# Kernel tuning notes

Measured on AMD Instinct MI355X. Metric: run time of the kernel, lower is better.

The kernel has to match this reference:

```python
import jax, jax.numpy as jnp
import numpy as np

EMBED_DIM = 1024
N_HEAD = 16
BLOCK_SIZE = 2048
B, T = 4, 2048


def setup_inputs() -> dict:
    key = jax.random.key(0)
    kx, kw, kb = jax.random.split(key, 3)
    x = jax.random.normal(kx, (B, T, EMBED_DIM), dtype=jnp.float32)
    # nn.Linear(embed_dim, 3*embed_dim): weight [3C, C], bias [3C]
    bound = 1.0 / np.sqrt(EMBED_DIM)
    W_qkv = jax.random.uniform(kw, (3 * EMBED_DIM, EMBED_DIM), dtype=jnp.float32, minval=-bound, maxval=bound)
    b_qkv = jax.random.uniform(kb, (3 * EMBED_DIM,), dtype=jnp.float32, minval=-bound, maxval=bound)
    return {"x": x, "W_qkv": W_qkv, "b_qkv": b_qkv}


def reference(x, W_qkv, b_qkv):
    Bsz, Tlen, C = x.shape
    H = N_HEAD
    hd = C // H
    qkv = x @ W_qkv.T + b_qkv  # [B, T, 3C]
    q, k, v = jnp.split(qkv, 3, axis=2)
    # [B, H, T, hd]
    q = q.reshape(Bsz, Tlen, H, hd).transpose(0, 2, 1, 3)
    k = k.reshape(Bsz, Tlen, H, hd).transpose(0, 2, 1, 3)
    v = v.reshape(Bsz, Tlen, H, hd).transpose(0, 2, 1, 3)
    att = jnp.einsum('bhqd,bhkd->bhqk', q, k) / np.sqrt(hd).astype(np.float32)
    causal = jnp.tril(jnp.ones((Tlen, Tlen), dtype=bool))
    att = jnp.where(causal[None, None, :, :], att, -jnp.inf)
    att = jax.nn.softmax(att, axis=-1)
    out = jnp.einsum('bhqk,bhkd->bhqd', att, v)  # [B, H, T, hd]
    y = out.transpose(0, 2, 1, 3).reshape(Bsz, Tlen, C)
    return y
```

## Files before the change

### kernel.cpp

```cpp
#include <hip/hip_runtime.h>


typedef unsigned short u16;
typedef short bf16x8 __attribute__((ext_vector_type(8)));
typedef float f32x4 __attribute__((ext_vector_type(4)));
typedef float f32x16 __attribute__((ext_vector_type(16)));

__device__ __forceinline__ float exp2f_hw(float x) {
  return __builtin_amdgcn_exp2f(x);
}

__device__ __forceinline__ u16 f2b(float f) {
  union { float f; unsigned u; } x; x.f = f;
  unsigned r = x.u + 0x7FFFu + ((x.u >> 16) & 1u);
  return (u16)(r >> 16);
}

__device__ __forceinline__ unsigned cvtpk(float lo, float hi_) {
  unsigned r;
  asm("v_cvt_pk_bf16_f32 %0, %1, %2" : "=v"(r) : "v"(lo), "v"(hi_));
  return r;
}

__device__ __forceinline__ void gload16(const void* g, void* l) {
  __builtin_amdgcn_global_load_lds(
      (const __attribute__((address_space(1))) unsigned*)g,
      (__attribute__((address_space(3))) unsigned*)l, 16, 0, 0);
}

__global__ void cvt_bf16(const float* __restrict__ src, u16* __restrict__ dst, int n4) {
  int i = blockIdx.x * blockDim.x + threadIdx.x;
  const int stride = gridDim.x * blockDim.x;
  for (; i < n4; i += stride) {
    float4 v = ((const float4*)src)[i];
    ushort4 o;
    o.x = f2b(v.x); o.y = f2b(v.y); o.z = f2b(v.z); o.w = f2b(v.w);
    ((ushort4*)dst)[i] = o;
  }
}

__global__ __launch_bounds__(256) void qkv_gemm(
    const u16* __restrict__ Xb, const u16* __restrict__ Wb,
    const float* __restrict__ bias,
    u16* __restrict__ qw, u16* __restrict__ kw, u16* __restrict__ vw) {
  __shared__ u16 As[8192];
  __shared__ u16 Bs[8192];
  const int tid  = threadIdx.x;
  const int lane = tid & 63;
  const int wave = tid >> 6;
  const int ln = lane & 15, hi = lane >> 4;
  const int wr = wave >> 1, wc = wave & 1;
  const int m0 = blockIdx.y * 128;
  const int n0 = blockIdx.x * 128;
  const bool vblk = (n0 >= 2048);

  const int srow = tid >> 2;
  const int scol = (tid & 3) * 8;

  f32x4 zero = {0.f, 0.f, 0.f, 0.f};
  f32x4 acc[4][4];
#pragma unroll
  for (int i = 0; i < 4; ++i)
#pragma unroll
    for (int j = 0; j < 4; ++j) acc[i][j] = zero;

  for (int k0 = 0; k0 < 1024; k0 += 64) {
    gload16(Xb + (size_t)(m0 + srow) * 1024 + k0 + scol,           (char*)As + tid * 16);
    gload16(Xb + (size_t)(m0 + 64 + srow) * 1024 + k0 + scol,      (char*)As + 4096 + tid * 16);
    gload16(Xb + (size_t)(m0 + srow) * 1024 + k0 + 32 + scol,      (char*)As + 8192 + tid * 16);
    gload16(Xb + (size_t)(m0 + 64 + srow) * 1024 + k0 + 32 + scol, (char*)As + 12288 + tid * 16);
    gload16(Wb + (size_t)(n0 + srow) * 1024 + k0 + scol,           (char*)Bs + tid * 16);
    gload16(Wb + (size_t)(n0 + 64 + srow) * 1024 + k0 + scol,      (char*)Bs + 4096 + tid * 16);
    gload16(Wb + (size_t)(n0 + srow) * 1024 + k0 + 32 + scol,      (char*)Bs + 8192 + tid * 16);
    gload16(Wb + (size_t)(n0 + 64 + srow) * 1024 + k0 + 32 + scol, (char*)Bs + 12288 + tid * 16);
    __syncthreads();

#pragma unroll
    for (int hf = 0; hf < 2; ++hf) {
      const u16* Ah = As + hf * 4096;
      const u16* Bh = Bs + hf * 4096;
      bf16x8 af[4], bfv[4];
#pragma unroll
      for (int i = 0; i < 4; ++i)
        af[i] = *(const bf16x8*)&Ah[(wr * 64 + i * 16 + ln) * 32 + hi * 8];
#pragma unroll
      for (int j = 0; j < 4; ++j)
        bfv[j] = *(const bf16x8*)&Bh[(wc * 64 + j * 16 + ln) * 32 + hi * 8];
      if (vblk) {
#pragma unroll
        for (int i = 0; i < 4; ++i)
#pragma unroll
          for (int j = 0; j < 4; ++j)
            acc[i][j] = __builtin_amdgcn_mfma_f32_16x16x32_bf16(bfv[j], af[i], acc[i][j], 0, 0, 0);
      } else {
#pragma unroll
        for (int i = 0; i < 4; ++i)
#pragma unroll
          for (int j = 0; j < 4; ++j)
            acc[i][j] = __builtin_amdgcn_mfma_f32_16x16x32_bf16(af[i], bfv[j], acc[i][j], 0, 0, 0);
      }
    }
    __syncthreads();
  }

  const int which = n0 >> 10;
  const int h = ((n0 & 1023) >> 6) + wc;
  const size_t bh = (size_t)((m0 >> 11) * 16 + h);
  const int tloc = (m0 & 2047) + wr * 64;

  if (which == 2) {
    u16* ob = vw + bh * 131072;
#pragma unroll
    for (int j = 0; j < 4; ++j) {
      float bv[4];
#pragma unroll
      for (int r = 0; r < 4; ++r) bv[r] = bias[n0 + wc * 64 + j * 16 + hi * 4 + r];
#pragma unroll
      for (int i = 0; i < 4; ++i) {
        u16* p = ob + (((tloc >> 4) + i) * 64 + j * 16 + hi * 4) * 16 + ln;
#pragma unroll
        for (int r = 0; r < 4; ++r)
          p[r * 16] = f2b(acc[i][j][r] + bv[r]);
      }
    }
  } else {
    u16* ob = (which == 0 ? qw : kw) + bh * 131072;
    const float qs = (which == 0) ? 0.1803368801111244f : 1.0f;
    const int t5 = tloc >> 5;
#pragma unroll
    for (int j = 0; j < 4; ++j) {
      const float bv = bias[n0 + wc * 64 + j * 16 + ln];
#pragma unroll
      for (int i = 0; i < 4; ++i) {
        u16* p = ob + ((t5 + (i >> 1)) * 4 + j) * 512 + ((i & 1) * 16 + hi * 4) * 16 + ln;
#pragma unroll
        for (int r = 0; r < 4; ++r)
          p[r * 16] = f2b((acc[i][j][r] + bv) * qs);
      }
    }
  }
}

__global__ __launch_bounds__(128) void attn(
    const u16* __restrict__ qw, const u16* __restrict__ kw,
    const u16* __restrict__ vw, float* __restrict__ y) {
  __shared__ float accX[2][16][64];
  __shared__ float lX[2][16][64];

  const int lane = threadIdx.x & 63;
  const int p    = threadIdx.x >> 6;
  const int l31 = lane & 31;
  const int hi  = lane >> 5;
  const int laneoff = l31 * 16 + hi * 8;

  const int bid = blockIdx.x;
  const int xcd = bid & 7;
  const int rest = bid >> 3;
  const int task = rest & 31;
  const int bh  = xcd + 8 * (rest >> 5);
  const int bb  = bh >> 4, h = bh & 15;

  const u16* qb = qw + (size_t)bh * 131072;
  const u16* kb = kw + (size_t)bh * 131072;
  const u16* vb = vw + (size_t)bh * 131072;
  float* yb = y + (size_t)bb * 2048 * 1024 + (size_t)h * 64;

  bf16x8 onesf;
#pragma unroll
  for (int j = 0; j < 8; ++j) onesf[j] = (short)0x3F80;

#pragma unroll 1
  for (int phase = 0; phase < 2; ++phase) {
    const int chunk = phase ? (63 - task) : task;
    const int q0 = chunk * 32;
    const int jtE = chunk;

    bf16x8 qf[4];
#pragma unroll
    for (int s = 0; s < 4; ++s)
      qf[s] = *(const bf16x8*)&qb[(chunk * 4 + s) * 512 + laneoff];

    f32x16 acc0, acc1, accl;
#pragma unroll
    for (int r = 0; r < 16; ++r) { acc0[r] = 0.f; acc1[r] = 0.f; accl[r] = 0.f; }

    bf16x8 kf[4];
#pragma unroll
    for (int s = 0; s < 4; ++s)
      kf[s] = *(const bf16x8*)&kb[(p * 4 + s) * 512 + laneoff];

#pragma unroll 1
    for (int jt = p; jt <= jtE; jt += 2) {
      bf16x8 vf[4];
      vf[0] = *(const bf16x8*)&vb[((jt * 2 + 0) * 64 +  0 + l31) * 16 + hi * 8];
      vf[1] = *(const bf16x8*)&vb[((jt * 2 + 0) * 64 + 32 + l31) * 16 + hi * 8];
      vf[2] = *(const bf16x8*)&vb[((jt * 2 + 1) * 64 +  0 + l31) * 16 + hi * 8];
      vf[3] = *(const bf16x8*)&vb[((jt * 2 + 1) * 64 + 32 + l31) * 16 + hi * 8];

      f32x16 st;
#pragma unroll
      for (int r = 0; r < 16; ++r) st[r] = 0.f;
#pragma unroll
      for (int s = 0; s < 4; ++s)
        st = __builtin_amdgcn_mfma_f32_32x32x16_bf16(kf[s], qf[s], st, 0, 0, 0);

      if (jt + 2 <= jtE) {
#pragma unroll
        for (int s = 0; s < 4; ++s)
          kf[s] = *(const bf16x8*)&kb[((jt + 2) * 4 + s) * 512 + laneoff];
      }

      if (jt == jtE) {
#pragma unroll
        for (int r = 0; r < 16; ++r) {
          const int crow = (r & 3) + 8 * (r >> 2) + 4 * hi;
          if (crow > l31) st[r] = -1e30f;
        }
      }

#pragma unroll
      for (int r = 0; r < 16; ++r) st[r] = exp2f_hw(fminf(st[r], 80.f));

      bf16x8 pa0, pa1;
      {
        unsigned x0 = cvtpk(st[0], st[1]),  y0 = cvtpk(st[4], st[5]);
        unsigned x1 = cvtpk(st[2], st[3]),  y1 = cvtpk(st[6], st[7]);
        auto s0 = __builtin_amdgcn_permlane32_swap(x0, y0, false, false);
        auto s1 = __builtin_amdgcn_permlane32_swap(x1, y1, false, false);
        union { unsigned w[4]; bf16x8 v; } u;
        u.w[0] = s0[0]; u.w[1] = s1[0]; u.w[2] = s0[1]; u.w[3] = s1[1];
        pa0 = u.v;
      }
      {
        unsigned x0 = cvtpk(st[8], st[9]),   y0 = cvtpk(st[12], st[13]);
        unsigned x1 = cvtpk(st[10], st[11]), y1 = cvtpk(st[14], st[15]);
        auto s0 = __builtin_amdgcn_permlane32_swap(x0, y0, false, false);
        auto s1 = __builtin_amdgcn_permlane32_swap(x1, y1, false, false);
        union { unsigned w[4]; bf16x8 v; } u;
        u.w[0] = s0[0]; u.w[1] = s1[0]; u.w[2] = s0[1]; u.w[3] = s1[1];
        pa1 = u.v;
      }

      acc0 = __builtin_amdgcn_mfma_f32_32x32x16_bf16(pa0, vf[0], acc0, 0, 0, 0);
      acc1 = __builtin_amdgcn_mfma_f32_32x32x16_bf16(pa0, vf[1], acc1, 0, 0, 0);
      accl = __builtin_amdgcn_mfma_f32_32x32x16_bf16(pa0, onesf, accl, 0, 0, 0);
      acc0 = __builtin_amdgcn_mfma_f32_32x32x16_bf16(pa1, vf[2], acc0, 0, 0, 0);
      acc1 = __builtin_amdgcn_mfma_f32_32x32x16_bf16(pa1, vf[3], acc1, 0, 0, 0);
      accl = __builtin_amdgcn_mfma_f32_32x32x16_bf16(pa1, onesf, accl, 0, 0, 0);
    }

    __syncthreads();
    if (p == 0) {
#pragma unroll
      for (int r = 0; r < 16; ++r) { accX[0][r][lane] = acc1[r]; lX[0][r][lane] = accl[r]; }
    } else {
#pragma unroll
      for (int r = 0; r < 16; ++r) { accX[1][r][lane] = acc0[r]; lX[1][r][lane] = accl[r]; }
    }
    __syncthreads();

#pragma unroll
    for (int r = 0; r < 16; ++r) {
      const int crow = (r & 3) + 8 * (r >> 2) + 4 * hi;
      const float own = (p == 0) ? acc0[r] : acc1[r];
      const float oth = accX[p ^ 1][r][lane];
      const float inv = 1.0f / (accl[r] + lX[p ^ 1][r][lane]);
      yb[(size_t)(q0 + crow) * 1024 + p * 32 + l31] = (own + oth) * inv;
    }
  }
}

extern "C" void kernel_launch(void* const* d_in, const int* in_sizes, int n_in,
                              void* d_out, int out_size, void* d_ws, size_t ws_size,
                              hipStream_t stream) {
  const float* x    = (const float*)d_in[0];
  const float* W    = (const float*)d_in[1];
  const float* bias = (const float*)d_in[2];
  float* y = (float*)d_out;

  char* ws = (char*)d_ws;
  u16* xb = (u16*)(ws);
  u16* Wb = (u16*)(ws + 16777216);
  u16* qw = (u16*)(ws + 23068672);
  u16* kw = (u16*)(ws + 39845888);
  u16* vw = (u16*)(ws + 56623104);

  cvt_bf16<<<2048, 256, 0, stream>>>(x, xb, 8388608 / 4);
  cvt_bf16<<<1024, 256, 0, stream>>>(W, Wb, 3145728 / 4);
  qkv_gemm<<<dim3(24, 64), 256, 0, stream>>>(xb, Wb, bias, qw, kw, vw);
  attn<<<2048, 128, 0, stream>>>(qw, kw, vw, y);
}
```

Before: 153.5 us.

## Process two 32-row query chunks per attention block to reuse K/V loads

The attention kernel now handles 64 query rows per phase, as two 32-row chunks A and B that share each loaded K and V tile. The grid is halved from 2048 to 1024 blocks. The goal is to halve K/V global loads per query row and give each wave more independent MFMA work to interleave. In exchange it roughly doubles accumulator register pressure, which may lower occupancy, and adds masked wasted work on the diagonal tile for chunk A.

After: 142.0 us. 7.5% less time.

```diff
diff --git a/kernel.cpp b/kernel.cpp
--- a/kernel.cpp
+++ b/kernel.cpp
@@ -26,6 +26,29 @@
   __builtin_amdgcn_global_load_lds(
       (const __attribute__((address_space(1))) unsigned*)g,
       (__attribute__((address_space(3))) unsigned*)l, 16, 0, 0);
+}
+
+__device__ __forceinline__ void packP(f32x16 st, bf16x8& pa0, bf16x8& pa1) {
+#pragma unroll
+  for (int r = 0; r < 16; ++r) st[r] = exp2f_hw(fminf(st[r], 80.f));
+  {
+    unsigned x0 = cvtpk(st[0], st[1]),  y0 = cvtpk(st[4], st[5]);
+    unsigned x1 = cvtpk(st[2], st[3]),  y1 = cvtpk(st[6], st[7]);
+    auto s0 = __builtin_amdgcn_permlane32_swap(x0, y0, false, false);
+    auto s1 = __builtin_amdgcn_permlane32_swap(x1, y1, false, false);
+    union { unsigned w[4]; bf16x8 v; } u;
+    u.w[0] = s0[0]; u.w[1] = s1[0]; u.w[2] = s0[1]; u.w[3] = s1[1];
+    pa0 = u.v;
+  }
+  {
+    unsigned x0 = cvtpk(st[8], st[9]),   y0 = cvtpk(st[12], st[13]);
+    unsigned x1 = cvtpk(st[10], st[11]), y1 = cvtpk(st[14], st[15]);
+    auto s0 = __builtin_amdgcn_permlane32_swap(x0, y0, false, false);
+    auto s1 = __builtin_amdgcn_permlane32_swap(x1, y1, false, false);
+    union { unsigned w[4]; bf16x8 v; } u;
+    u.w[0] = s0[0]; u.w[1] = s1[0]; u.w[2] = s0[1]; u.w[3] = s1[1];
+    pa1 = u.v;
+  }
 }
 
 __global__ void cvt_bf16(const float* __restrict__ src, u16* __restrict__ dst, int n4) {
@@ -144,8 +167,10 @@
 __global__ __launch_bounds__(128) void attn(
     const u16* __restrict__ qw, const u16* __restrict__ kw,
     const u16* __restrict__ vw, float* __restrict__ y) {
-  __shared__ float accX[2][16][64];
-  __shared__ float lX[2][16][64];
+  __shared__ float accXA[2][16][64];
+  __shared__ float lXA[2][16][64];
+  __shared__ float accXB[2][16][64];
+  __shared__ float lXB[2][16][64];
 
   const int lane = threadIdx.x & 63;
   const int p    = threadIdx.x >> 6;
@@ -156,8 +181,8 @@
   const int bid = blockIdx.x;
   const int xcd = bid & 7;
   const int rest = bid >> 3;
-  const int task = rest & 31;
-  const int bh  = xcd + 8 * (rest >> 5);
+  const int pr  = rest & 15;
+  const int bh  = xcd + 8 * (rest >> 4);
   const int bb  = bh >> 4, h = bh & 15;
 
   const u16* qb = qw + (size_t)bh * 131072;
@@ -171,23 +196,29 @@
 
 #pragma unroll 1
   for (int phase = 0; phase < 2; ++phase) {
-    const int chunk = phase ? (63 - task) : task;
-    const int q0 = chunk * 32;
-    const int jtE = chunk;
-
-    bf16x8 qf[4];
-#pragma unroll
-    for (int s = 0; s < 4; ++s)
-      qf[s] = *(const bf16x8*)&qb[(chunk * 4 + s) * 512 + laneoff];
-
-    f32x16 acc0, acc1, accl;
-#pragma unroll
-    for (int r = 0; r < 16; ++r) { acc0[r] = 0.f; acc1[r] = 0.f; accl[r] = 0.f; }
+    const int s  = phase ? (31 - pr) : pr;
+    const int q0 = s * 64;
+    const int cA = 2 * s, cB = 2 * s + 1;
+    const int jtE = cB;
+
+    bf16x8 qfA[4], qfB[4];
+#pragma unroll
+    for (int sb = 0; sb < 4; ++sb) {
+      qfA[sb] = *(const bf16x8*)&qb[(cA * 4 + sb) * 512 + laneoff];
+      qfB[sb] = *(const bf16x8*)&qb[(cB * 4 + sb) * 512 + laneoff];
+    }
+
+    f32x16 accA0, accA1, acclA, accB0, accB1, acclB;
+#pragma unroll
+    for (int r = 0; r < 16; ++r) {
+      accA0[r] = 0.f; accA1[r] = 0.f; acclA[r] = 0.f;
+      accB0[r] = 0.f; accB1[r] = 0.f; acclB[r] = 0.f;
+    }
 
     bf16x8 kf[4];
 #pragma unroll
-    for (int s = 0; s < 4; ++s)
-      kf[s] = *(const bf16x8*)&kb[(p * 4 + s) * 512 + laneoff];
+    for (int sb = 0; sb < 4; ++sb)
+      kf[sb] = *(const bf16x8*)&kb[(p * 4 + sb) * 512 + laneoff];
 
 #pragma unroll 1
     for (int jt = p; jt <= jtE; jt += 2) {
@@ -197,75 +228,82 @@
       vf[2] = *(const bf16x8*)&vb[((jt * 2 + 1) * 64 +  0 + l31) * 16 + hi * 8];
       vf[3] = *(const bf16x8*)&vb[((jt * 2 + 1) * 64 + 32 + l31) * 16 + hi * 8];
 
-      f32x16 st;
-#pragma unroll
-      for (int r = 0; r < 16; ++r) st[r] = 0.f;
-#pragma unroll
-      for (int s = 0; s < 4; ++s)
-        st = __builtin_amdgcn_mfma_f32_32x32x16_bf16(kf[s], qf[s], st, 0, 0, 0);
-
+      f32x16 stA, stB;
+#pragma unroll
+      for (int r = 0; r < 16; ++r) { stA[r] = 0.f; stB[r] = 0.f; }
+#pragma unroll
+      for (int sb = 0; sb < 4; ++sb) {
+        stA = __builtin_amdgcn_mfma_f32_32x32x16_bf16(kf[sb], qfA[sb], stA, 0, 0, 0);
+        stB = __builtin_amdgcn_mfma_f32_32x32x16_bf16(kf[sb], qfB[sb], stB, 0, 0, 0);
+      }
       if (jt + 2 <= jtE) {
 #pragma unroll
-        for (int s = 0; s < 4; ++s)
-          kf[s] = *(const bf16x8*)&kb[((jt + 2) * 4 + s) * 512 + laneoff];
-      }
-
-      if (jt == jtE) {
+        for (int sb = 0; sb < 4; ++sb)
+          kf[sb] = *(const bf16x8*)&kb[((jt + 2) * 4 + sb) * 512 + laneoff];
+      }
+
+      if (jt == cA) {
 #pragma unroll
         for (int r = 0; r < 16; ++r) {
           const int crow = (r & 3) + 8 * (r >> 2) + 4 * hi;
-          if (crow > l31) st[r] = -1e30f;
+          if (crow > l31) stA[r] = -1e30f;
         }
       }
-
-#pragma unroll
-      for (int r = 0; r < 16; ++r) st[r] = exp2f_hw(fminf(st[r], 80.f));
+      if (jt == cB) {
+#pragma unroll
+        for (int r = 0; r < 16; ++r) {
+          const int crow = (r & 3) + 8 * (r >> 2) + 4 * hi;
+          stA[r] = -1e30f;
+          if (crow > l31) stB[r] = -1e30f;
+        }
+      }
 
       bf16x8 pa0, pa1;
-      {
-        unsigned x0 = cvtpk(st[0], st[1]),  y0 = cvtpk(st[4], st[5]);
-        unsigned x1 = cvtpk(st[2], st[3]),  y1 = cvtpk(st[6], st[7]);
-        auto s0 = __builtin_amdgcn_permlane32_swap(x0, y0, false, false);
-        auto s1 = __builtin_amdgcn_permlane32_swap(x1, y1, false, false);
-        union { unsigned w[4]; bf16x8 v; } u;
-        u.w[0] = s0[0]; u.w[1] = s1[0]; u.w[2] = s0[1]; u.w[3] = s1[1];
-        pa0 = u.v;
-      }
-      {
-        unsigned x0 = cvtpk(st[8], st[9]),   y0 = cvtpk(st[12], st[13]);
-        unsigned x1 = cvtpk(st[10], st[11]), y1 = cvtpk(st[14], st[15]);
-        auto s0 = __builtin_amdgcn_permlane32_swap(x0, y0, false, false);
-        auto s1 = __builtin_amdgcn_permlane32_swap(x1, y1, false, false);
-        union { unsigned w[4]; bf16x8 v; } u;
-        u.w[0] = s0[0]; u.w[1] = s1[0]; u.w[2] = s0[1]; u.w[3] = s1[1];
-        pa1 = u.v;
-      }
-
-      acc0 = __builtin_amdgcn_mfma_f32_32x32x16_bf16(pa0, vf[0], acc0, 0, 0, 0);
-      acc1 = __builtin_amdgcn_mfma_f32_32x32x16_bf16(pa0, vf[1], acc1, 0, 0, 0);
-      accl = __builtin_amdgcn_mfma_f32_32x32x16_bf16(pa0, onesf, accl, 0, 0, 0);
-      acc0 = __builtin_amdgcn_mfma_f32_32x32x16_bf16(pa1, vf[2], acc0, 0, 0, 0);
-      acc1 = __builtin_amdgcn_mfma_f32_32x32x16_bf16(pa1, vf[3], acc1, 0, 0, 0);
-      accl = __builtin_amdgcn_mfma_f32_32x32x16_bf16(pa1, onesf, accl, 0, 0, 0);
+      packP(stA, pa0, pa1);
+      accA0 = __builtin_amdgcn_mfma_f32_32x32x16_bf16(pa0, vf[0], accA0, 0, 0, 0);
+      accA1 = __builtin_amdgcn_mfma_f32_32x32x16_bf16(pa0, vf[1], accA1, 0, 0, 0);
+      acclA = __builtin_amdgcn_mfma_f32_32x32x16_bf16(pa0, onesf, acclA, 0, 0, 0);
+      accA0 = __builtin_amdgcn_mfma_f32_32x32x16_bf16(pa1, vf[2], accA0, 0, 0, 0);
+      accA1 = __builtin_amdgcn_mfma_f32_32x32x16_bf16(pa1, vf[3], accA1, 0, 0, 0);
+      acclA = __builtin_amdgcn_mfma_f32_32x32x16_bf16(pa1, onesf, acclA, 0, 0, 0);
+
+      packP(stB, pa0, pa1);
+      accB0 = __builtin_amdgcn_mfma_f32_32x32x16_bf16(pa0, vf[0], accB0, 0, 0, 0);
+      accB1 = __builtin_amdgcn_mfma_f32_32x32x16_bf16(pa0, vf[1], accB1, 0, 0, 0);
+      acclB = __builtin_amdgcn_mfma_f32_32x32x16_bf16(pa0, onesf, acclB, 0, 0, 0);
+      accB0 = __builtin_amdgcn_mfma_f32_32x32x16_bf16(pa1, vf[2], accB0, 0, 0, 0);
+      accB1 = __builtin_amdgcn_mfma_f32_32x32x16_bf16(pa1, vf[3], accB1, 0, 0, 0);
+      acclB = __builtin_amdgcn_mfma_f32_32x32x16_bf16(pa1, onesf, acclB, 0, 0, 0);
     }
 
     __syncthreads();
     if (p == 0) {
 #pragma unroll
-      for (int r = 0; r < 16; ++r) { accX[0][r][lane] = acc1[r]; lX[0][r][lane] = accl[r]; }
+      for (int r = 0; r < 16; ++r) {
+        accXA[0][r][lane] = accA1[r]; lXA[0][r][lane] = acclA[r];
+        accXB[0][r][lane] = accB1[r]; lXB[0][r][lane] = acclB[r];
+      }
     } else {
 #pragma unroll
-      for (int r = 0; r < 16; ++r) { accX[1][r][lane] = acc0[r]; lX[1][r][lane] = accl[r]; }
+      for (int r = 0; r < 16; ++r) {
+        accXA[1][r][lane] = accA0[r]; lXA[1][r][lane] = acclA[r];
+        accXB[1][r][lane] = accB0[r]; lXB[1][r][lane] = acclB[r];
+      }
     }
     __syncthreads();
 
 #pragma unroll
     for (int r = 0; r < 16; ++r) {
       const int crow = (r & 3) + 8 * (r >> 2) + 4 * hi;
-      const float own = (p == 0) ? acc0[r] : acc1[r];
-      const float oth = accX[p ^ 1][r][lane];
-      const float inv = 1.0f / (accl[r] + lX[p ^ 1][r][lane]);
-      yb[(size_t)(q0 + crow) * 1024 + p * 32 + l31] = (own + oth) * inv;
+      const float ownA = (p == 0) ? accA0[r] : accA1[r];
+      const float othA = accXA[p ^ 1][r][lane];
+      const float invA = 1.0f / (acclA[r] + lXA[p ^ 1][r][lane]);
+      yb[(size_t)(q0 + crow) * 1024 + p * 32 + l31] = (ownA + othA) * invA;
+
+      const float ownB = (p == 0) ? accB0[r] : accB1[r];
+      const float othB = accXB[p ^ 1][r][lane];
+      const float invB = 1.0f / (acclB[r] + lXB[p ^ 1][r][lane]);
+      yb[(size_t)(q0 + 32 + crow) * 1024 + p * 32 + l31] = (ownB + othB) * invB;
     }
   }
 }
@@ -288,5 +326,5 @@
   cvt_bf16<<<2048, 256, 0, stream>>>(x, xb, 8388608 / 4);
   cvt_bf16<<<1024, 256, 0, stream>>>(W, Wb, 3145728 / 4);
   qkv_gemm<<<dim3(24, 64), 256, 0, stream>>>(xb, Wb, bias, qw, kw, vw);
-  attn<<<2048, 128, 0, stream>>>(qw, kw, vw, y);
-}
+  attn<<<1024, 128, 0, stream>>>(qw, kw, vw, y);
+}
```
